# Performance work log

Hardware: AMD Instinct MI355X
Metric: run time of the kernel (lower is better)

Reference implementation:

```python
import jax, jax.numpy as jnp
import numpy as np

L, C, H, DH, LAT, N, B = 6, 768, 12, 64, 256, 65, 512


def setup_inputs() -> dict:
    key = jax.random.key(0)
    ks = jax.random.split(key, 16)
    def p(k, shape, std=0.02):
        return jax.random.normal(k, shape, jnp.float32) * std
    return {
        "x": jax.random.normal(ks[0], (B, N, C), jnp.float32),
        "ln1_g": jnp.ones((L, C), jnp.float32), "ln1_b": jnp.zeros((L, C), jnp.float32),
        "qkv_w": p(ks[1], (L, C, 3 * C)),
        "proj_w": p(ks[2], (L, C, C)),
        "qn_g": jnp.ones((L, DH), jnp.float32), "qn_b": jnp.zeros((L, DH), jnp.float32),
        "kn_g": jnp.ones((L, DH), jnp.float32), "kn_b": jnp.zeros((L, DH), jnp.float32),
        "sg_w1": p(ks[3], (L, C, 2 * LAT)),
        "sg_ln1_g": jnp.ones((L, 2 * LAT), jnp.float32), "sg_ln1_b": jnp.zeros((L, 2 * LAT), jnp.float32),
        "sg_w2": p(ks[4], (L, 2 * LAT, LAT * H)),
        "sg_ln2_g": jnp.ones((L, LAT * H), jnp.float32), "sg_ln2_b": jnp.zeros((L, LAT * H), jnp.float32),
        "sg_bias_w": p(ks[5], (L, LAT, 65 * 65), std=0.005),
        "ln2_g": jnp.ones((L, C), jnp.float32), "ln2_b": jnp.zeros((L, C), jnp.float32),
        "gate_w": p(ks[6], (L, C, 4 * C)),
        "value_w": p(ks[7], (L, C, 4 * C)),
        "out_w": p(ks[8], (L, 4 * C, C)),
    }


def _ln(x, g, b, eps=1e-5):
    # torch nn.LayerNorm: biased variance
    m = jnp.mean(x, axis=-1, keepdims=True)
    v = jnp.var(x, axis=-1, keepdims=True)
    return (x - m) * jax.lax.rsqrt(v + eps) * g + b


def _block(x, p):
    (l1g, l1b, qkvw, projw, qng, qnb, kng, knb,
     w1, s1g, s1b, w2, s2g, s2b, bw, l2g, l2b, gw, vw, ow) = p
    Bb, Nn, Cc = x.shape
    scale = DH ** -0.5
    h = _ln(x, l1g, l1b)
    cls = h[:, 0]                                     # (B, C)
    qkv = (h @ qkvw).reshape(Bb, Nn, 3, H, DH).transpose(2, 0, 3, 1, 4)
    q, k, v = qkv[0], qkv[1], qkv[2]                  # each (B, H, N, DH)
    q = _ln(q, qng, qnb) * scale
    k = _ln(k, kng, knb)
    attn = jnp.einsum('bhnd,bhmd->bhnm', q, k)        # (B, H, N, N)
    # SmolGen: CLS -> per-head additive bias
    lat1 = jax.nn.silu(_ln(cls @ w1, s1g, s1b))       # (B, 2*LAT)
    lat2 = _ln(lat1 @ w2, s2g, s2b).reshape(Bb, H, LAT)
    bias = (lat2 @ bw).reshape(Bb, H, 65, 65)
    attn = jax.nn.softmax(attn + bias[:, :, :Nn, :Nn], axis=-1)
    o = jnp.einsum('bhnm,bhmd->bhnd', attn, v)
    o = o.transpose(0, 2, 1, 3).reshape(Bb, Nn, Cc)
    x = x + o @ projw
    h2 = _ln(x, l2g, l2b)
    x = x + ((h2 @ gw) * jax.nn.silu(h2 @ vw)) @ ow   # SwiGLU
    return x, None


def reference(x, ln1_g, ln1_b, qkv_w, proj_w, qn_g, qn_b, kn_g, kn_b,
              sg_w1, sg_ln1_g, sg_ln1_b, sg_w2, sg_ln2_g, sg_ln2_b, sg_bias_w,
              ln2_g, ln2_b, gate_w, value_w, out_w):
    params = (ln1_g, ln1_b, qkv_w, proj_w, qn_g, qn_b, kn_g, kn_b,
              sg_w1, sg_ln1_g, sg_ln1_b, sg_w2, sg_ln2_g, sg_ln2_b, sg_bias_w,
              ln2_g, ln2_b, gate_w, value_w, out_w)
    out, _ = jax.lax.scan(_block, x, params)
    return out
```

## Files before the change

kernel.cpp:

```cpp
#include <hip/hip_runtime.h>
#include <hip/hip_bf16.h>


typedef __bf16 v8bf  __attribute__((ext_vector_type(8)));
typedef __bf16 v4bf  __attribute__((ext_vector_type(4)));
typedef float  v16f  __attribute__((ext_vector_type(16)));

#define EPI_BF16      0
#define EPI_ADDF32    1
#define EPI_SILU      2
#define EPI_MUL       3
#define EPI_BF16MASK  4

__device__ __forceinline__ v16f mfma32(v8bf a, v8bf b, v16f c) {
  return __builtin_amdgcn_mfma_f32_32x32x16_bf16(a, b, c, 0, 0, 0);
}

template<int EPI>
__global__ __launch_bounds__(256, 3)
void gemm_bt(const __bf16* __restrict__ A, long long lda,
             const __bf16* __restrict__ Bt,
             void* outp, const __bf16* extra,
             int Nout, int K, int nvalid)
{
  __shared__ __align__(16) __bf16 Als[128 * 64];
  __shared__ __align__(16) __bf16 Bls[128 * 64];
  const int tid  = threadIdx.x;
  const int w    = tid >> 6, lane = tid & 63;
  const int m0   = blockIdx.y * 128, n0 = blockIdx.x * 128;
  const int wm   = (w & 1) * 64, wn = (w >> 1) * 64;
  const int l31  = lane & 31, l5 = lane >> 5;

  const __bf16* ag[4];
  const __bf16* bg[4];
#pragma unroll
  for (int i = 0; i < 4; ++i) {
    int li  = i * 256 + tid;
    int row = li >> 3;
    int c   = (li & 7) ^ (row & 7);
    ag[i] = A  + (size_t)(m0 + row) * (size_t)lda + c * 8;
    bg[i] = Bt + (size_t)(n0 + row) * (size_t)K   + c * 8;
  }
  char* alds0 = ((char*)Als) + w * 1024;
  char* blds0 = ((char*)Bls) + w * 1024;

  v16f acc[2][2] = {};

  for (int kt = 0; kt < K; kt += 64) {
#pragma unroll
    for (int i = 0; i < 4; ++i) {
      __builtin_amdgcn_global_load_lds(
          (const __attribute__((address_space(1))) void*)(ag[i]),
          (__attribute__((address_space(3))) void*)(alds0 + i * 4096), 16, 0, 0);
      __builtin_amdgcn_global_load_lds(
          (const __attribute__((address_space(1))) void*)(bg[i]),
          (__attribute__((address_space(3))) void*)(blds0 + i * 4096), 16, 0, 0);
      ag[i] += 64; bg[i] += 64;
    }
    __syncthreads();
#pragma unroll
    for (int kk = 0; kk < 4; ++kk) {
      v8bf af[2], bf[2];
#pragma unroll
      for (int t = 0; t < 2; ++t) {
        int m  = wm + t * 32 + l31;
        int ch = (kk * 2 + l5) ^ (m & 7);
        af[t] = *(const v8bf*)(Als + m * 64 + ch * 8);
        int n   = wn + t * 32 + l31;
        int ch2 = (kk * 2 + l5) ^ (n & 7);
        bf[t] = *(const v8bf*)(Bls + n * 64 + ch2 * 8);
      }
      acc[0][0] = mfma32(af[0], bf[0], acc[0][0]);
      acc[0][1] = mfma32(af[0], bf[1], acc[0][1]);
      acc[1][0] = mfma32(af[1], bf[0], acc[1][0]);
      acc[1][1] = mfma32(af[1], bf[1], acc[1][1]);
    }
    __syncthreads();
  }

#pragma unroll
  for (int mi = 0; mi < 2; ++mi)
#pragma unroll
  for (int ni = 0; ni < 2; ++ni) {
    int col  = n0 + wn + ni * 32 + l31;
    int rowb = m0 + wm + mi * 32 + 4 * l5;
#pragma unroll
    for (int r = 0; r < 16; ++r) {
      int row   = rowb + (r & 3) + 8 * (r >> 2);
      float val = acc[mi][ni][r];
      size_t idx = (size_t)row * (size_t)Nout + col;
      if (EPI == EPI_BF16) {
        ((__bf16*)outp)[idx] = (__bf16)val;
      } else if (EPI == EPI_ADDF32) {
        ((float*)outp)[idx] += val;
      } else if (EPI == EPI_SILU) {
        float s = val / (1.f + __expf(-val));
        ((__bf16*)outp)[idx] = (__bf16)s;
      } else if (EPI == EPI_MUL) {
        float e = (float)extra[idx];
        ((__bf16*)outp)[idx] = (__bf16)(val * e);
      } else {
        int stride = (nvalid + 7) & ~7;
        if (col < nvalid)
          ((__bf16*)outp)[(size_t)row * (size_t)stride + col] = (__bf16)val;
      }
    }
  }
}

__global__ void transpose_w(const float* __restrict__ src, __bf16* __restrict__ dst,
                            int K, int N, int Npad)
{
  __shared__ float t[32][33];
  int n0 = blockIdx.x * 32, k0 = blockIdx.y * 32;
  int tx = threadIdx.x, ty = threadIdx.y;
#pragma unroll
  for (int i = 0; i < 32; i += 8) {
    int k = k0 + ty + i, n = n0 + tx;
    t[ty + i][tx] = (k < K && n < N) ? src[(size_t)k * N + n] : 0.f;
  }
  __syncthreads();
#pragma unroll
  for (int i = 0; i < 32; i += 8) {
    int n = n0 + ty + i, k = k0 + tx;
    if (n < Npad && k < K) dst[(size_t)n * K + k] = (__bf16)t[tx][ty + i];
  }
}

__global__ __launch_bounds__(256)
void ln768_f32_to_bf16(const float* __restrict__ x, const float* __restrict__ g,
                       const float* __restrict__ bb, __bf16* __restrict__ out)
{
  const int row  = blockIdx.x * 4 + (threadIdx.x >> 6);
  const int lane = threadIdx.x & 63;
  const float* xr = x + (size_t)row * 768;
  float4 v[3];
  float sum = 0.f, sq = 0.f;
#pragma unroll
  for (int c = 0; c < 3; ++c) {
    v[c] = *(const float4*)(xr + c * 256 + lane * 4);
    sum += v[c].x + v[c].y + v[c].z + v[c].w;
    sq  += v[c].x * v[c].x + v[c].y * v[c].y + v[c].z * v[c].z + v[c].w * v[c].w;
  }
#pragma unroll
  for (int d = 1; d < 64; d <<= 1) { sum += __shfl_xor(sum, d); sq += __shfl_xor(sq, d); }
  float mean = sum * (1.f / 768.f);
  float var  = sq * (1.f / 768.f) - mean * mean;
  float rs   = rsqrtf(var + 1e-5f);
  __bf16* orow = out + (size_t)row * 768;
#pragma unroll
  for (int c = 0; c < 3; ++c) {
    float4 gv = *(const float4*)(g  + c * 256 + lane * 4);
    float4 bv = *(const float4*)(bb + c * 256 + lane * 4);
    v4bf o4;
    o4[0] = (__bf16)((v[c].x - mean) * rs * gv.x + bv.x);
    o4[1] = (__bf16)((v[c].y - mean) * rs * gv.y + bv.y);
    o4[2] = (__bf16)((v[c].z - mean) * rs * gv.z + bv.z);
    o4[3] = (__bf16)((v[c].w - mean) * rs * gv.w + bv.w);
    *(v4bf*)(orow + c * 256 + lane * 4) = o4;
  }
}

__global__ __launch_bounds__(256)
void ln_bf16_kernel(const __bf16* __restrict__ x, const float* __restrict__ g,
                    const float* __restrict__ bb, __bf16* __restrict__ out,
                    int C, int do_silu)
{
  __shared__ float sm[8];
  const __bf16* xr = x + (size_t)blockIdx.x * C;
  float sum = 0.f, sq = 0.f;
  for (int i = threadIdx.x; i < C; i += 256) { float v = (float)xr[i]; sum += v; sq += v * v; }
#pragma unroll
  for (int d = 1; d < 64; d <<= 1) { sum += __shfl_xor(sum, d); sq += __shfl_xor(sq, d); }
  if ((threadIdx.x & 63) == 0) { sm[threadIdx.x >> 6] = sum; sm[4 + (threadIdx.x >> 6)] = sq; }
  __syncthreads();
  sum = sm[0] + sm[1] + sm[2] + sm[3];
  sq  = sm[4] + sm[5] + sm[6] + sm[7];
  float mean = sum / C;
  float var  = sq / C - mean * mean;
  float rs   = rsqrtf(var + 1e-5f);
  __bf16* orow = out + (size_t)blockIdx.x * C;
  for (int i = threadIdx.x; i < C; i += 256) {
    float y = ((float)xr[i] - mean) * rs * g[i] + bb[i];
    if (do_silu) y = y / (1.f + __expf(-y));
    orow[i] = (__bf16)y;
  }
}

__global__ __launch_bounds__(256)
void attn_mfma(const __bf16* __restrict__ qkv,
               const float* __restrict__ qg, const float* __restrict__ qb,
               const float* __restrict__ kg, const float* __restrict__ kb,
               const __bf16* __restrict__ bias, __bf16* __restrict__ o)
{
  __shared__ __align__(16) char smem[49424];
  __bf16* qs = (__bf16*)smem;
  __bf16* ks = (__bf16*)(smem + 12288);
  __bf16* Ps = (__bf16*)smem;
  __bf16* vt = (__bf16*)(smem + 24576);
  __bf16* bl = (__bf16*)(smem + 40960);

  const int tid = threadIdx.x;
  const int bh  = blockIdx.x;
  const int b = bh / 12, h = bh % 12;
  const int w = tid >> 6, lane = tid & 63;
  const int l31 = lane & 31, l5 = lane >> 5;
  const int li = lane & 7, rg = lane >> 3;

  const __bf16* bp = bias + (size_t)bh * 4232;
  for (int idx = tid; idx < 529; idx += 256)
    *(v8bf*)(bl + idx * 8) = *(const v8bf*)(bp + idx * 8);

  float qgv[8], qbv[8], kgv[8], kbv[8];
#pragma unroll
  for (int e = 0; e < 8; ++e) {
    qgv[e] = qg[li * 8 + e]; qbv[e] = qb[li * 8 + e];
    kgv[e] = kg[li * 8 + e]; kbv[e] = kb[li * 8 + e];
  }

  for (int n0 = 0; n0 < 65; n0 += 32) {
    int n = n0 + w * 8 + rg;
    if (n < 65) {
      const __bf16* src = qkv + ((size_t)(b * 65 + n)) * 2304 + h * 64 + li * 8;
      v8bf qv8 = *(const v8bf*)(src);
      v8bf kv8 = *(const v8bf*)(src + 768);
      v8bf vv8 = *(const v8bf*)(src + 1536);
      float qf[8], kf[8];
      float s1 = 0.f, s2 = 0.f, t1 = 0.f, t2 = 0.f;
#pragma unroll
      for (int e = 0; e < 8; ++e) {
        qf[e] = (float)qv8[e]; kf[e] = (float)kv8[e];
        s1 += qf[e]; s2 += qf[e] * qf[e];
        t1 += kf[e]; t2 += kf[e] * kf[e];
      }
#pragma unroll
      for (int d = 1; d < 8; d <<= 1) {
        s1 += __shfl_xor(s1, d); s2 += __shfl_xor(s2, d);
        t1 += __shfl_xor(t1, d); t2 += __shfl_xor(t2, d);
      }
      float qm = s1 * 0.015625f, qva = s2 * 0.015625f - qm * qm;
      float km = t1 * 0.015625f, kva = t2 * 0.015625f - km * km;
      float qrs = rsqrtf(qva + 1e-5f), krs = rsqrtf(kva + 1e-5f);
      v8bf qo, ko;
#pragma unroll
      for (int e = 0; e < 8; ++e) {
        qo[e] = (__bf16)(((qf[e] - qm) * qrs * qgv[e] + qbv[e]) * 0.125f);
        ko[e] = (__bf16)((kf[e] - km) * krs * kgv[e] + kbv[e]);
      }
      *(v8bf*)(qs + n * 64 + (li ^ (n & 7)) * 8) = qo;
      *(v8bf*)(ks + n * 64 + (li ^ (n & 7)) * 8) = ko;
#pragma unroll
      for (int e = 0; e < 8; ++e) {
        int d = li * 8 + e;
        int swz = (d & 7) ^ (d >> 3);
        vt[d * 128 + (((n >> 3) ^ swz) * 8) + (n & 7)] = vv8[e];
      }
    }
  }
  for (int e2 = tid; e2 < 64 * 31; e2 += 256) {
    int d = e2 / 31, j = 65 + e2 % 31;
    int swz = (d & 7) ^ (d >> 3);
    vt[d * 128 + (((j >> 3) ^ swz) * 8) + (j & 7)] = (__bf16)0.f;
  }
  __syncthreads();

  v16f s0 = {}, s1v = {}, s2v = {};
  if (w < 3) {
    const int mrow = w * 32 + l31;
#pragma unroll
    for (int kk = 0; kk < 4; ++kk) {
      int lc = kk * 2 + l5;
      v8bf aq = *(const v8bf*)(qs + mrow * 64 + ((lc ^ (mrow & 7)) * 8));
      v8bf b0 = *(const v8bf*)(ks + (l31) * 64      + ((lc ^ ((l31) & 7)) * 8));
      v8bf b1 = *(const v8bf*)(ks + (32 + l31) * 64 + ((lc ^ ((32 + l31) & 7)) * 8));
      v8bf b2 = *(const v8bf*)(ks + (64 + l31) * 64 + ((lc ^ ((64 + l31) & 7)) * 8));
      s0  = mfma32(aq, b0, s0);
      s1v = mfma32(aq, b1, s1v);
      s2v = mfma32(aq, b2, s2v);
    }
  }
  __syncthreads();

  if (w < 3) {
    const int j0 = l31, j1 = 32 + l31, j2 = 64 + l31;
#pragma unroll
    for (int r = 0; r < 16; ++r) {
      int i = w * 32 + 4 * l5 + (r & 3) + 8 * (r >> 2);
      float v0 = s0[r], v1 = s1v[r], v2 = s2v[r];
      if (i < 65) {
        v0 += (float)bl[i * 65 + j0];
        v1 += (float)bl[i * 65 + j1];
        if (l31 == 0) v2 += (float)bl[i * 65 + 64];
      }
      float vx = (l31 == 0) ? v2 : -1e30f;
      float mx = fmaxf(fmaxf(v0, v1), vx);
#pragma unroll
      for (int d = 1; d < 32; d <<= 1) mx = fmaxf(mx, __shfl_xor(mx, d));
      float e0 = __expf(v0 - mx);
      float e1 = __expf(v1 - mx);
      float e2 = (l31 == 0) ? __expf(v2 - mx) : 0.f;
      float sum = e0 + e1 + e2;
#pragma unroll
      for (int d = 1; d < 32; d <<= 1) sum += __shfl_xor(sum, d);
      float inv = 1.f / sum;
      Ps[i * 128 + (((j0 >> 3) ^ (i & 7)) * 8) + (j0 & 7)] = (__bf16)(e0 * inv);
      Ps[i * 128 + (((j1 >> 3) ^ (i & 7)) * 8) + (j1 & 7)] = (__bf16)(e1 * inv);
      Ps[i * 128 + (((j2 >> 3) ^ (i & 7)) * 8) + (j2 & 7)] =
          (__bf16)((l31 == 0) ? e2 * inv : 0.f);
    }
  }
  __syncthreads();

  const int nt = (w < 2) ? 2 : 1;
  for (int tt = 0; tt < nt; ++tt) {
    int t = w + tt * 4;
    int it = t >> 1, dt = t & 1;
    int prow = it * 32 + l31;
    int drow = dt * 32 + l31;
    int dswz = (drow & 7) ^ (drow >> 3);
    v16f acc = {};
#pragma unroll
    for (int kk = 0; kk < 6; ++kk) {
      int lc = kk * 2 + l5;
      v8bf ap = *(const v8bf*)(Ps + prow * 128 + ((lc ^ (prow & 7)) * 8));
      v8bf bv = *(const v8bf*)(vt + drow * 128 + ((lc ^ dswz) * 8));
      acc = mfma32(ap, bv, acc);
    }
    int dcol = dt * 32 + l31;
#pragma unroll
    for (int r = 0; r < 16; ++r) {
      int i = it * 32 + 4 * l5 + (r & 3) + 8 * (r >> 2);
      if (i < 65)
        o[((size_t)(b * 65 + i) * 12 + h) * 64 + dcol] = (__bf16)acc[r];
    }
  }
}

extern "C" void kernel_launch(void* const* d_in, const int* in_sizes, int n_in,
                              void* d_out, int out_size, void* d_ws, size_t ws_size,
                              hipStream_t stream)
{
  (void)in_sizes; (void)n_in; (void)ws_size;
  const float* x_in    = (const float*)d_in[0];
  const float* ln1_g   = (const float*)d_in[1];
  const float* ln1_b   = (const float*)d_in[2];
  const float* qkv_w   = (const float*)d_in[3];
  const float* proj_w  = (const float*)d_in[4];
  const float* qn_g    = (const float*)d_in[5];
  const float* qn_b    = (const float*)d_in[6];
  const float* kn_g    = (const float*)d_in[7];
  const float* kn_b    = (const float*)d_in[8];
  const float* sg_w1   = (const float*)d_in[9];
  const float* sg_ln1g = (const float*)d_in[10];
  const float* sg_ln1b = (const float*)d_in[11];
  const float* sg_w2   = (const float*)d_in[12];
  const float* sg_ln2g = (const float*)d_in[13];
  const float* sg_ln2b = (const float*)d_in[14];
  const float* sg_bw   = (const float*)d_in[15];
  const float* ln2_g   = (const float*)d_in[16];
  const float* ln2_b   = (const float*)d_in[17];
  const float* gate_w  = (const float*)d_in[18];
  const float* value_w = (const float*)d_in[19];
  const float* out_w   = (const float*)d_in[20];

  char* ws = (char*)d_ws;
  size_t off = 0;
  auto alloc = [&](size_t bytes) -> char* {
    char* p = ws + off; off += (bytes + 255) & ~(size_t)255; return p;
  };

  __bf16* wt_qkv  = (__bf16*)alloc(2304ull * 768 * 2);
  __bf16* wt_proj = (__bf16*)alloc(768ull * 768 * 2);
  __bf16* wt_sg1  = (__bf16*)alloc(512ull * 768 * 2);
  __bf16* wt_sg2  = (__bf16*)alloc(3072ull * 512 * 2);
  __bf16* wt_bias = (__bf16*)alloc(4352ull * 256 * 2);
  __bf16* wt_gate = (__bf16*)alloc(3072ull * 768 * 2);
  __bf16* wt_val  = (__bf16*)alloc(3072ull * 768 * 2);
  __bf16* wt_out  = (__bf16*)alloc(768ull * 3072 * 2);
  __bf16* hbuf    = (__bf16*)alloc(33280ull * 768 * 2);
  __bf16* biasbuf = (__bf16*)alloc(6144ull * 4232 * 2);
  __bf16* BIG     = (__bf16*)alloc(33280ull * 2304 * 2);
  __bf16* t1buf   = (__bf16*)alloc(512ull * 512 * 2);
  __bf16* lat1    = (__bf16*)alloc(512ull * 512 * 2);
  __bf16* t2buf   = (__bf16*)alloc(512ull * 3072 * 2);
  __bf16* lat2    = (__bf16*)alloc(512ull * 3072 * 2);

  __bf16* qkvbuf = BIG;
  __bf16* mlpbuf = biasbuf;

  hipMemcpyAsync(d_out, x_in, (size_t)out_size * sizeof(float),
                 hipMemcpyDeviceToDevice, stream);
  float* xb = (float*)d_out;

  dim3 tb(32, 8);
  for (int l = 0; l < 6; ++l) {
    const float* l1g = ln1_g + l * 768;
    const float* l1b = ln1_b + l * 768;
    const float* qg  = qn_g + l * 64;
    const float* qb  = qn_b + l * 64;
    const float* kg  = kn_g + l * 64;
    const float* kb  = kn_b + l * 64;
    const float* s1g = sg_ln1g + l * 512;
    const float* s1b = sg_ln1b + l * 512;
    const float* s2g = sg_ln2g + l * 3072;
    const float* s2b = sg_ln2b + l * 3072;
    const float* l2g = ln2_g + l * 768;
    const float* l2b = ln2_b + l * 768;

    transpose_w<<<dim3(72, 24), tb, 0, stream>>>(qkv_w  + (size_t)l * 768 * 2304, wt_qkv, 768, 2304, 2304);
    transpose_w<<<dim3(24, 24), tb, 0, stream>>>(proj_w + (size_t)l * 768 * 768,  wt_proj, 768, 768, 768);
    transpose_w<<<dim3(16, 24), tb, 0, stream>>>(sg_w1  + (size_t)l * 768 * 512,  wt_sg1, 768, 512, 512);
    transpose_w<<<dim3(96, 16), tb, 0, stream>>>(sg_w2  + (size_t)l * 512 * 3072, wt_sg2, 512, 3072, 3072);
    transpose_w<<<dim3(136, 8), tb, 0, stream>>>(sg_bw  + (size_t)l * 256 * 4225, wt_bias, 256, 4225, 4352);
    transpose_w<<<dim3(96, 24), tb, 0, stream>>>(gate_w + (size_t)l * 768 * 3072, wt_gate, 768, 3072, 3072);
    transpose_w<<<dim3(96, 24), tb, 0, stream>>>(value_w+ (size_t)l * 768 * 3072, wt_val, 768, 3072, 3072);
    transpose_w<<<dim3(24, 96), tb, 0, stream>>>(out_w  + (size_t)l * 3072 * 768, wt_out, 3072, 768, 768);

    ln768_f32_to_bf16<<<8320, 256, 0, stream>>>(xb, l1g, l1b, hbuf);
    gemm_bt<EPI_BF16><<<dim3(18, 260), 256, 0, stream>>>(
        hbuf, 768, wt_qkv, qkvbuf, nullptr, 2304, 768, 2304);
    gemm_bt<EPI_BF16><<<dim3(4, 4), 256, 0, stream>>>(
        hbuf, 65 * 768, wt_sg1, t1buf, nullptr, 512, 768, 512);
    ln_bf16_kernel<<<512, 256, 0, stream>>>(t1buf, s1g, s1b, lat1, 512, 1);
    gemm_bt<EPI_BF16><<<dim3(24, 4), 256, 0, stream>>>(
        lat1, 512, wt_sg2, t2buf, nullptr, 3072, 512, 3072);
    ln_bf16_kernel<<<512, 256, 0, stream>>>(t2buf, s2g, s2b, lat2, 3072, 0);
    gemm_bt<EPI_BF16MASK><<<dim3(34, 48), 256, 0, stream>>>(
        lat2, 256, wt_bias, biasbuf, nullptr, 4352, 256, 4225);
    attn_mfma<<<6144, 256, 0, stream>>>(qkvbuf, qg, qb, kg, kb, biasbuf, hbuf);
    gemm_bt<EPI_ADDF32><<<dim3(6, 260), 256, 0, stream>>>(
        hbuf, 768, wt_proj, xb, nullptr, 768, 768, 768);
    ln768_f32_to_bf16<<<8320, 256, 0, stream>>>(xb, l2g, l2b, hbuf);
    gemm_bt<EPI_SILU><<<dim3(24, 260), 256, 0, stream>>>(
        hbuf, 768, wt_val, mlpbuf, nullptr, 3072, 768, 3072);
    gemm_bt<EPI_MUL><<<dim3(24, 260), 256, 0, stream>>>(
        hbuf, 768, wt_gate, mlpbuf, mlpbuf, 3072, 768, 3072);
    gemm_bt<EPI_ADDF32><<<dim3(6, 260), 256, 0, stream>>>(
        mlpbuf, 3072, wt_out, xb, nullptr, 768, 3072, 768);
  }
}
```

Before: 8.208 ms.

## Fuse SwiGLU GEMMs, batch weight transposes, remap GEMM blocks across XCDs

Replaces the separate value-SiLU and gate-multiply GEMMs with one kernel that loads the activation tile once and accumulates both products, removing a full write and re-read of the 3072-wide MLP buffer. It also merges the eight per-layer weight transpose launches into one batched launch and adds an XCD-aware block-index remap to the GEMMs so neighbouring tiles share an L2. The generic GEMM's occupancy hint rises from 3 to 5 waves. The fused kernel doubles accumulator registers and uses more LDS, which may lower occupancy.

```diff
diff --git a/kernel.cpp b/kernel.cpp
--- a/kernel.cpp
+++ b/kernel.cpp
@@ -16,8 +16,18 @@
   return __builtin_amdgcn_mfma_f32_32x32x16_bf16(a, b, c, 0, 0, 0);
 }
 
+__device__ __forceinline__ void xcd_remap(int& bx, int& by) {
+  const int gx = gridDim.x;
+  const int nwg = gx * gridDim.y;
+  int id = by * gx + bx;
+  int q = nwg >> 3, r = nwg & 7;
+  int xcd = id & 7, pos = id >> 3;
+  int nid = (xcd < r ? xcd * (q + 1) : r * (q + 1) + (xcd - r) * q) + pos;
+  bx = nid % gx; by = nid / gx;
+}
+
 template<int EPI>
-__global__ __launch_bounds__(256, 3)
+__global__ __launch_bounds__(256, 5)
 void gemm_bt(const __bf16* __restrict__ A, long long lda,
              const __bf16* __restrict__ Bt,
              void* outp, const __bf16* extra,
@@ -27,7 +37,9 @@
   __shared__ __align__(16) __bf16 Bls[128 * 64];
   const int tid  = threadIdx.x;
   const int w    = tid >> 6, lane = tid & 63;
-  const int m0   = blockIdx.y * 128, n0 = blockIdx.x * 128;
+  int bx = blockIdx.x, by = blockIdx.y;
+  xcd_remap(bx, by);
+  const int m0   = by * 128, n0 = bx * 128;
   const int wm   = (w & 1) * 64, wn = (w >> 1) * 64;
   const int l31  = lane & 31, l5 = lane >> 5;
 
@@ -108,11 +120,117 @@
   }
 }
 
-__global__ void transpose_w(const float* __restrict__ src, __bf16* __restrict__ dst,
-                            int K, int N, int Npad)
+__global__ __launch_bounds__(256, 3)
+void gemm_mlp(const __bf16* __restrict__ A,
+              const __bf16* __restrict__ Bv, const __bf16* __restrict__ Bg,
+              __bf16* __restrict__ outp, int Nout, int K)
+{
+  __shared__ __align__(16) __bf16 Als [128 * 64];
+  __shared__ __align__(16) __bf16 Bvls[128 * 64];
+  __shared__ __align__(16) __bf16 Bgls[128 * 64];
+  const int tid  = threadIdx.x;
+  const int w    = tid >> 6, lane = tid & 63;
+  int bx = blockIdx.x, by = blockIdx.y;
+  xcd_remap(bx, by);
+  const int m0   = by * 128, n0 = bx * 128;
+  const int wm   = (w & 1) * 64, wn = (w >> 1) * 64;
+  const int l31  = lane & 31, l5 = lane >> 5;
+
+  const __bf16* ag[4];
+  const __bf16* bvg[4];
+  const __bf16* bgg[4];
+#pragma unroll
+  for (int i = 0; i < 4; ++i) {
+    int li  = i * 256 + tid;
+    int row = li >> 3;
+    int c   = (li & 7) ^ (row & 7);
+    ag[i]  = A  + (size_t)(m0 + row) * (size_t)K + c * 8;
+    bvg[i] = Bv + (size_t)(n0 + row) * (size_t)K + c * 8;
+    bgg[i] = Bg + (size_t)(n0 + row) * (size_t)K + c * 8;
+  }
+  char* alds0  = ((char*)Als)  + w * 1024;
+  char* bvlds0 = ((char*)Bvls) + w * 1024;
+  char* bglds0 = ((char*)Bgls) + w * 1024;
+
+  v16f accv[2][2] = {};
+  v16f accg[2][2] = {};
+
+  for (int kt = 0; kt < K; kt += 64) {
+#pragma unroll
+    for (int i = 0; i < 4; ++i) {
+      __builtin_amdgcn_global_load_lds(
+          (const __attribute__((address_space(1))) void*)(ag[i]),
+          (__attribute__((address_space(3))) void*)(alds0 + i * 4096), 16, 0, 0);
+      __builtin_amdgcn_global_load_lds(
+          (const __attribute__((address_space(1))) void*)(bvg[i]),
+          (__attribute__((address_space(3))) void*)(bvlds0 + i * 4096), 16, 0, 0);
+      __builtin_amdgcn_global_load_lds(
+          (const __attribute__((address_space(1))) void*)(bgg[i]),
+          (__attribute__((address_space(3))) void*)(bglds0 + i * 4096), 16, 0, 0);
+      ag[i] += 64; bvg[i] += 64; bgg[i] += 64;
+    }
+    __syncthreads();
+#pragma unroll
+    for (int kk = 0; kk < 4; ++kk) {
+      v8bf af[2], bv[2], bg2[2];
+#pragma unroll
+      for (int t = 0; t < 2; ++t) {
+        int m  = wm + t * 32 + l31;
+        int ch = (kk * 2 + l5) ^ (m & 7);
+        af[t] = *(const v8bf*)(Als + m * 64 + ch * 8);
+        int n   = wn + t * 32 + l31;
+        int ch2 = (kk * 2 + l5) ^ (n & 7);
+        bv[t]  = *(const v8bf*)(Bvls + n * 64 + ch2 * 8);
+        bg2[t] = *(const v8bf*)(Bgls + n * 64 + ch2 * 8);
+      }
+      accv[0][0] = mfma32(af[0], bv[0],  accv[0][0]);
+      accg[0][0] = mfma32(af[0], bg2[0], accg[0][0]);
+      accv[0][1] = mfma32(af[0], bv[1],  accv[0][1]);
+      accg[0][1] = mfma32(af[0], bg2[1], accg[0][1]);
+      accv[1][0] = mfma32(af[1], bv[0],  accv[1][0]);
+      accg[1][0] = mfma32(af[1], bg2[0], accg[1][0]);
+      accv[1][1] = mfma32(af[1], bv[1],  accv[1][1]);
+      accg[1][1] = mfma32(af[1], bg2[1], accg[1][1]);
+    }
+    __syncthreads();
+  }
+
+#pragma unroll
+  for (int mi = 0; mi < 2; ++mi)
+#pragma unroll
+  for (int ni = 0; ni < 2; ++ni) {
+    int col  = n0 + wn + ni * 32 + l31;
+    int rowb = m0 + wm + mi * 32 + 4 * l5;
+#pragma unroll
+    for (int r = 0; r < 16; ++r) {
+      int row = rowb + (r & 3) + 8 * (r >> 2);
+      float v = accv[mi][ni][r];
+      float g = accg[mi][ni][r];
+      float s = v / (1.f + __expf(-v)) * g;
+      outp[(size_t)row * (size_t)Nout + col] = (__bf16)s;
+    }
+  }
+}
+
+struct TBatch {
+  const float* src[8];
+  __bf16* dst[8];
+  int K[8], N[8], Npad[8], gx[8], blk0[8];
+};
+
+__global__ void transpose_batched(TBatch tb)
 {
   __shared__ float t[32][33];
-  int n0 = blockIdx.x * 32, k0 = blockIdx.y * 32;
+  int id = blockIdx.x;
+  int s = 0;
+#pragma unroll
+  for (int i = 1; i < 8; ++i) if (id >= tb.blk0[i]) s = i;
+  const float* src = tb.src[s];
+  __bf16* dst = tb.dst[s];
+  const int K = tb.K[s], N = tb.N[s], Npad = tb.Npad[s];
+  int local = id - tb.blk0[s];
+  int bx = local % tb.gx[s], by = local / tb.gx[s];
+  int n0 = bx * 32, k0 = by * 32;
   int tx = threadIdx.x, ty = threadIdx.y;
 #pragma unroll
   for (int i = 0; i < 32; i += 8) {
@@ -407,14 +525,26 @@
     const float* l2g = ln2_g + l * 768;
     const float* l2b = ln2_b + l * 768;
 
-    transpose_w<<<dim3(72, 24), tb, 0, stream>>>(qkv_w  + (size_t)l * 768 * 2304, wt_qkv, 768, 2304, 2304);
-    transpose_w<<<dim3(24, 24), tb, 0, stream>>>(proj_w + (size_t)l * 768 * 768,  wt_proj, 768, 768, 768);
-    transpose_w<<<dim3(16, 24), tb, 0, stream>>>(sg_w1  + (size_t)l * 768 * 512,  wt_sg1, 768, 512, 512);
-    transpose_w<<<dim3(96, 16), tb, 0, stream>>>(sg_w2  + (size_t)l * 512 * 3072, wt_sg2, 512, 3072, 3072);
-    transpose_w<<<dim3(136, 8), tb, 0, stream>>>(sg_bw  + (size_t)l * 256 * 4225, wt_bias, 256, 4225, 4352);
-    transpose_w<<<dim3(96, 24), tb, 0, stream>>>(gate_w + (size_t)l * 768 * 3072, wt_gate, 768, 3072, 3072);
-    transpose_w<<<dim3(96, 24), tb, 0, stream>>>(value_w+ (size_t)l * 768 * 3072, wt_val, 768, 3072, 3072);
-    transpose_w<<<dim3(24, 96), tb, 0, stream>>>(out_w  + (size_t)l * 3072 * 768, wt_out, 3072, 768, 768);
+    TBatch tbat;
+    const float* srcs[8] = {
+      qkv_w  + (size_t)l * 768 * 2304, proj_w + (size_t)l * 768 * 768,
+      sg_w1  + (size_t)l * 768 * 512,  sg_w2  + (size_t)l * 512 * 3072,
+      sg_bw  + (size_t)l * 256 * 4225, gate_w + (size_t)l * 768 * 3072,
+      value_w+ (size_t)l * 768 * 3072, out_w  + (size_t)l * 3072 * 768 };
+    __bf16* dsts[8] = { wt_qkv, wt_proj, wt_sg1, wt_sg2, wt_bias,
+                        wt_gate, wt_val, wt_out };
+    const int Ks[8]  = {768, 768, 768, 512, 256, 768, 768, 3072};
+    const int Ns[8]  = {2304, 768, 512, 3072, 4225, 3072, 3072, 768};
+    const int Nps[8] = {2304, 768, 512, 3072, 4352, 3072, 3072, 768};
+    int blk = 0;
+    for (int s = 0; s < 8; ++s) {
+      tbat.src[s] = srcs[s]; tbat.dst[s] = dsts[s];
+      tbat.K[s] = Ks[s]; tbat.N[s] = Ns[s]; tbat.Npad[s] = Nps[s];
+      tbat.gx[s] = Nps[s] / 32;
+      tbat.blk0[s] = blk;
+      blk += (Nps[s] / 32) * ((Ks[s] + 31) / 32);
+    }
+    transpose_batched<<<blk, tb, 0, stream>>>(tbat);
 
     ln768_f32_to_bf16<<<8320, 256, 0, stream>>>(xb, l1g, l1b, hbuf);
     gemm_bt<EPI_BF16><<<dim3(18, 260), 256, 0, stream>>>(
@@ -431,10 +561,8 @@
     gemm_bt<EPI_ADDF32><<<dim3(6, 260), 256, 0, stream>>>(
         hbuf, 768, wt_proj, xb, nullptr, 768, 768, 768);
     ln768_f32_to_bf16<<<8320, 256, 0, stream>>>(xb, l2g, l2b, hbuf);
-    gemm_bt<EPI_SILU><<<dim3(24, 260), 256, 0, stream>>>(
-        hbuf, 768, wt_val, mlpbuf, nullptr, 3072, 768, 3072);
-    gemm_bt<EPI_MUL><<<dim3(24, 260), 256, 0, stream>>>(
-        hbuf, 768, wt_gate, mlpbuf, mlpbuf, 3072, 768, 3072);
+    gemm_mlp<<<dim3(24, 260), 256, 0, stream>>>(
+        hbuf, wt_val, wt_gate, mlpbuf, 3072, 768);
     gemm_bt<EPI_ADDF32><<<dim3(6, 260), 256, 0, stream>>>(
         mlpbuf, 3072, wt_out, xb, nullptr, 768, 3072, 768);
   }
```

Result: slower. 9.481 ms (+15.5%).
